# Kernel optimization log

Measured on AMD Instinct MI355X. Metric: run time of the kernel, lower is better.

The kernel has to match this reference:

```python
import jax, jax.numpy as jnp
import numpy as np

B, MB, NB, C = 4, 4096, 16384, 64

def setup_inputs() -> dict:
    key = jax.random.key(0)
    k1, k2, k3 = jax.random.split(key, 3)
    xyz = jax.random.normal(k1, (B * MB, 3), dtype=jnp.float32) * 10.0
    new_xyz = jax.random.normal(k2, (B * NB, 3), dtype=jnp.float32) * 10.0
    features = jax.random.normal(k3, (B * MB, C), dtype=jnp.float32)
    xyz_batch_cnt = jnp.full((B,), MB, dtype=jnp.int32)
    new_xyz_batch_cnt = jnp.full((B,), NB, dtype=jnp.int32)
    return {
        "xyz": xyz,
        "xyz_batch_cnt": xyz_batch_cnt,
        "new_xyz": new_xyz,
        "new_xyz_batch_cnt": new_xyz_batch_cnt,
        "features": features,
    }

def _three_nn_interp(query, known, feats):
    # query: (Nb,3), known: (Mb,3), feats: (Mb,C)
    # squared pairwise distances (Nb, Mb)
    d2 = (jnp.sum(query * query, -1, keepdims=True)
          - 2.0 * (query @ known.T)
          + jnp.sum(known * known, -1)[None, :])
    neg_d2, idx = jax.lax.top_k(-d2, 3)            # 3 nearest, (Nb,3)
    dist = jnp.sqrt(jnp.maximum(-neg_d2, 0.0))      # OpenPCDet returns sqrt(dist2)
    dist_recip = 1.0 / (dist + 1e-8)
    weight = dist_recip / jnp.sum(dist_recip, -1, keepdims=True)  # (Nb,3)
    gathered = feats[idx]                           # (Nb,3,C)
    return jnp.einsum('nkc,nk->nc', gathered, weight)

def reference(xyz, xyz_batch_cnt, new_xyz, new_xyz_batch_cnt, features):
    b = xyz_batch_cnt.shape[0]
    mb = xyz.shape[0] // b
    nb = new_xyz.shape[0] // b
    known_b = xyz.reshape(b, mb, 3)
    query_b = new_xyz.reshape(b, nb, 3)
    feats_b = features.reshape(b, mb, -1)
    out = jax.vmap(_three_nn_interp)(query_b, known_b, feats_b)  # (B,Nb,C)
    return out.reshape(b * nb, -1)
```

## Files before the change

kernel.cpp:

```cpp
#include <hip/hip_runtime.h>
#include <math.h>

#define NBIN   512
#define BEXT   64.0f
#define WSLACK 0.02f
#define AWIN   4.0f
#define BTH1   1024

__device__ __forceinline__ int bin1(float x) {
    int c = (int)floorf((x + BEXT) * 4.0f);
    return min(NBIN - 1, max(0, c));
}
__device__ __forceinline__ unsigned f2sort(float f) {
    int b = __float_as_int(f);
    return (unsigned)b ^ (0x80000000u | (unsigned)(b >> 31));
}
__device__ __forceinline__ float sort2f(unsigned u) {
    unsigned b = (u & 0x80000000u) ? (u ^ 0x80000000u) : ~u;
    return __uint_as_float(b);
}
__device__ __forceinline__ void ins3k(unsigned long long k,
                                      unsigned long long& k0,
                                      unsigned long long& k1,
                                      unsigned long long& k2) {
    const bool c0 = k < k0, c1 = k < k1, c2 = k < k2;
    k2 = c1 ? k1 : (c2 ? k : k2);
    k1 = c0 ? k0 : (c1 ? k : k1);
    k0 = c0 ? k  : k0;
}
__device__ __forceinline__ unsigned long long shfl_xor_u64(unsigned long long v, int m) {
    unsigned lo = (unsigned)v, hi = (unsigned)(v >> 32);
    lo = __shfl_xor((int)lo, m, 64);
    hi = __shfl_xor((int)hi, m, 64);
    return ((unsigned long long)hi << 32) | lo;
}

extern "C" __global__ void __launch_bounds__(BTH1)
build1d(const float* __restrict__ xyz, const float* __restrict__ nxyz,
        int mb, int nb,
        float4* __restrict__ ps, int* __restrict__ pidx,
        int* __restrict__ qord, int* __restrict__ boff,
        int* __restrict__ ovf_cnt)
{
    __shared__ int hist[NBIN];
    __shared__ int scanb[NBIN];
    const int B    = (int)gridDim.x / 2;
    const bool isQ = (int)blockIdx.x >= B;
    const int b    = isQ ? (int)blockIdx.x - B : (int)blockIdx.x;
    const int tid  = threadIdx.x;
    const int n    = isQ ? nb : mb;
    const float* P = (isQ ? nxyz : xyz) + (size_t)b * n * 3;

    if (blockIdx.x == 0 && tid < B) ovf_cnt[tid] = 0;

    if (tid < NBIN) hist[tid] = 0;
    __syncthreads();
    for (int i = tid; i < n; i += BTH1) atomicAdd(&hist[bin1(P[i * 3])], 1);
    __syncthreads();
    int h = 0;
    if (tid < NBIN) { h = hist[tid]; scanb[tid] = h; }
    __syncthreads();
    for (int off = 1; off < NBIN; off <<= 1) {
        int t = 0;
        if (tid < NBIN && tid >= off) t = scanb[tid - off];
        __syncthreads();
        if (tid < NBIN) scanb[tid] += t;
        __syncthreads();
    }
    if (tid < NBIN) {
        const int excl = scanb[tid] - h;
        if (!isQ) {
            boff[(size_t)b * (NBIN + 1) + tid] = excl;
            if (tid == NBIN - 1) boff[(size_t)b * (NBIN + 1) + NBIN] = n;
        }
        hist[tid] = excl;
    }
    __syncthreads();
    for (int i = tid; i < n; i += BTH1) {
        const float x = P[i * 3], y = P[i * 3 + 1], z = P[i * 3 + 2];
        const int c = bin1(x);
        const int pos = atomicAdd(&hist[c], 1);
        if (isQ) {
            qord[(size_t)b * nb + pos] = i;
        } else {
            float pn;
            {
#pragma clang fp contract(off)
                pn = (x * x + y * y) + z * z;
            }
            ps[(size_t)b * mb + pos]   = make_float4(x, y, z, pn);
            pidx[(size_t)b * mb + pos] = i;
        }
    }
}

#define QWA  8
#define SWA  8
#define WVBA 4
#define WTHA (WVBA * 64)
#define QPBA (WVBA * QWA)
#define CHA  64

extern "C" __global__ void __launch_bounds__(WTHA)
knn_phaseA(const float* __restrict__ nxyz, const float* __restrict__ feats,
           const int* __restrict__ qord, const int* __restrict__ boff,
           const float4* __restrict__ ps, const int* __restrict__ pidx,
           float* __restrict__ out, int* __restrict__ ovf, float* __restrict__ ovf_ub,
           int* __restrict__ ovf_cnt, int mb, int nb, int C)
{
    __shared__ float4 sP[WVBA][CHA];
    __shared__ int    sI[WVBA][CHA];

    const int tid  = threadIdx.x;
    const int w    = tid >> 6;
    const int l    = tid & 63;
    const int qi   = l & 7;
    const int side = l >> 3;
    const int wid  = blockIdx.x * WVBA + w;
    const int q0   = wid * QWA;
    const int b    = q0 / nb;

    const int qloc = qord[q0 + qi];
    const int row  = b * nb + qloc;
    const float qx = nxyz[(size_t)row * 3 + 0];
    const float qy = nxyz[(size_t)row * 3 + 1];
    const float qz = nxyz[(size_t)row * 3 + 2];
    float qq;
    {
#pragma clang fp contract(off)
        qq = (qx * qx + qy * qy) + qz * qz;
    }

    float mn = qx, mx = qx;
#pragma unroll
    for (int m = 1; m < 64; m <<= 1) {
        mn = fminf(mn, __shfl_xor(mn, m, 64));
        mx = fmaxf(mx, __shfl_xor(mx, m, 64));
    }

    const int*    boffb = boff + (size_t)b * (NBIN + 1);
    const float4* psb   = ps   + (size_t)b * mb;
    const int*    pib   = pidx + (size_t)b * mb;

    unsigned long long k0 = ~0ull, k1 = ~0ull, k2 = ~0ull;

    float4 rP;
    int    rI = 0;
    bool   rV = false;
    auto issue = [&](int base, int hi) {
        const int cand = base + l;
        rV = cand < hi;
        if (rV) { rP = psb[cand]; rI = pib[cand]; }
    };
    auto commit = [&]() {
        if (rV) { sP[w][l] = rP; sI[w][l] = rI; }
    };
    auto process = [&](int cnt) {
#pragma unroll
        for (int u = 0; u < CHA / SWA; ++u) {
            const int j = side + u * SWA;
            if (j < cnt) {
                const float4 Pt = sP[w][j];
                const int    pi = sI[w][j];
                const float dot = fmaf(qz, Pt.z, fmaf(qy, Pt.y, qx * Pt.x));
                const float d2  = fmaf(-2.0f, dot, qq) + Pt.w;
                const unsigned long long key =
                    ((unsigned long long)f2sort(d2) << 32) | (unsigned)pi;
                if (key < k2) {
                    const bool c0 = key < k0, c1 = key < k1;
                    k2 = c1 ? k1 : key;
                    k1 = c0 ? k0 : (c1 ? key : k1);
                    k0 = c0 ? key : k0;
                }
            }
        }
    };

    const int blo = bin1(mn - AWIN);
    const int bhi = bin1(mx + AWIN);
    {
        const int lo = boffb[blo], hi = boffb[bhi + 1];
        if (lo < hi) {
            issue(lo, hi);
            for (int base = lo; base < hi; base += CHA) {
                commit();
                if (base + CHA < hi) issue(base + CHA, hi);
                process(min(CHA, hi - base));
            }
        }
    }

    unsigned long long m0 = k0, m1 = k1, m2 = k2;
#pragma unroll
    for (int mk = 8; mk <= 32; mk <<= 1) {
        const unsigned long long t0 = shfl_xor_u64(m0, mk);
        const unsigned long long t1 = shfl_xor_u64(m1, mk);
        const unsigned long long t2 = shfl_xor_u64(m2, mk);
        ins3k(t0, m0, m1, m2); ins3k(t1, m0, m1, m2); ins3k(t2, m0, m1, m2);
    }

    const unsigned h2 = (unsigned)(m2 >> 32);
    const float ub = (h2 == 0xFFFFFFFFu) ? INFINITY : sort2f(h2);
    const float eL = fmaf(0.25f, (float)blo, -BEXT);
    const float eR = fmaf(0.25f, (float)(bhi + 1), -BEXT);
    const float gL = qx - eL;
    const float gR = eR - qx;
    const bool okL = (blo == 0)        || (gL * gL > ub + WSLACK);
    const bool okR = (bhi >= NBIN - 1) || (gR * gR > ub + WSLACK);
    const bool resolved = okL && okR && (h2 != 0xFFFFFFFFu);

    const bool need = (side == 0) && !resolved;
    const unsigned long long bm = __ballot(need);
    if (bm) {
        const int rank = __popcll(bm & ((1ull << l) - 1ull));
        const int tot  = __popcll(bm);
        const int lead = __ffsll((unsigned long long)bm) - 1;
        int base = 0;
        if (l == lead) base = atomicAdd(&ovf_cnt[b], tot);
        base = __shfl(base, lead, 64);
        if (need) {
            ovf[(size_t)b * nb + base + rank]    = row;
            ovf_ub[(size_t)b * nb + base + rank] = ub;
        }
    }

    const float d0  = sort2f((unsigned)(m0 >> 32));
    const float d1  = sort2f((unsigned)(m1 >> 32));
    const float d2v = sort2f((unsigned)(m2 >> 32));
    const float da = sqrtf(fmaxf(d0, 0.0f));
    const float db = sqrtf(fmaxf(d1, 0.0f));
    const float dc = sqrtf(fmaxf(d2v, 0.0f));
    const float ra = 1.0f / (da + 1e-8f);
    const float rb = 1.0f / (db + 1e-8f);
    const float rc = 1.0f / (dc + 1e-8f);
    float rs;
    {
#pragma clang fp contract(off)
        rs = (ra + rb) + rc;
    }
    const float wa = ra / rs, wb = rb / rs, wc = rc / rs;
    const int   ia = b * mb + (int)(unsigned)(m0 & 0xFFFFFFFFu);
    const int   ib = b * mb + (int)(unsigned)(m1 & 0xFFFFFFFFu);
    const int   ic = b * mb + (int)(unsigned)(m2 & 0xFFFFFFFFu);

    for (int q = 0; q < QWA; ++q) {
        if (__shfl((int)resolved, q, 64) == 0) continue;
        const float wa_ = __shfl(wa, q, 64);
        const float wb_ = __shfl(wb, q, 64);
        const float wc_ = __shfl(wc, q, 64);
        const int   ia_ = __shfl(ia, q, 64);
        const int   ib_ = __shfl(ib, q, 64);
        const int   ic_ = __shfl(ic, q, 64);
        const int   rw_ = __shfl(row, q, 64);
        const size_t ga = (size_t)ia_ * C;
        const size_t gb = (size_t)ib_ * C;
        const size_t gc = (size_t)ic_ * C;
        const size_t go = (size_t)rw_ * C;
        for (int ch = l; ch < C; ch += 64) {
            out[go + ch] = wa_ * feats[ga + ch] + wb_ * feats[gb + ch] + wc_ * feats[gc + ch];
        }
    }
}

#define WPBB 8
#define BTH2 (WPBB * 64)

extern "C" __global__ void __launch_bounds__(BTH2)
knn_phaseB2(const float* __restrict__ nxyz, const float* __restrict__ feats,
            const int* __restrict__ ovf, const float* __restrict__ ovf_ub,
            const int* __restrict__ ovf_cnt, const int* __restrict__ boff,
            const float4* __restrict__ ps, const int* __restrict__ pidx,
            float* __restrict__ out, int mb, int nb, int C)
{
    const int tid  = threadIdx.x;
    const int w    = tid >> 6;
    const int l    = tid & 63;
    const int bpb  = nb / WPBB;
    const int bb   = (int)blockIdx.x / bpb;
    const int slot = ((int)blockIdx.x % bpb) * WPBB + w;
    const int cnt  = ovf_cnt[bb];
    if (slot >= cnt) return;

    const int   row = ovf[(size_t)bb * nb + slot];
    const float ub  = ovf_ub[(size_t)bb * nb + slot];
    const float qx = nxyz[(size_t)row * 3 + 0];
    const float qy = nxyz[(size_t)row * 3 + 1];
    const float qz = nxyz[(size_t)row * 3 + 2];
    float qq;
    {
#pragma clang fp contract(off)
        qq = (qx * qx + qy * qy) + qz * qz;
    }

    int blo = 0, bhi = NBIN - 1;
    if (ub < 1e30f) {
        const float r = sqrtf(ub + 2.0f * WSLACK);
        blo = bin1(qx - r);
        bhi = bin1(qx + r);
    }
    const int*    boffb = boff + (size_t)bb * (NBIN + 1);
    const float4* psb   = ps   + (size_t)bb * mb;
    const int*    pib   = pidx + (size_t)bb * mb;
    const int lo = boffb[blo], hi = boffb[bhi + 1];

    unsigned long long k0 = ~0ull, k1 = ~0ull, k2 = ~0ull;
#pragma unroll 4
    for (int t = lo + l; t < hi; t += 64) {
        const float4 Pt = psb[t];
        const int    pi = pib[t];
        const float dot = fmaf(qz, Pt.z, fmaf(qy, Pt.y, qx * Pt.x));
        const float d2  = fmaf(-2.0f, dot, qq) + Pt.w;
        const unsigned long long key =
            ((unsigned long long)f2sort(d2) << 32) | (unsigned)pi;
        if (key < k2) {
            const bool c0 = key < k0, c1 = key < k1;
            k2 = c1 ? k1 : key;
            k1 = c0 ? k0 : (c1 ? key : k1);
            k0 = c0 ? key : k0;
        }
    }

#pragma unroll
    for (int m = 1; m < 64; m <<= 1) {
        const unsigned long long t0 = shfl_xor_u64(k0, m);
        const unsigned long long t1 = shfl_xor_u64(k1, m);
        const unsigned long long t2 = shfl_xor_u64(k2, m);
        ins3k(t0, k0, k1, k2); ins3k(t1, k0, k1, k2); ins3k(t2, k0, k1, k2);
    }

    const float d0  = sort2f((unsigned)(k0 >> 32));
    const float d1  = sort2f((unsigned)(k1 >> 32));
    const float d2v = sort2f((unsigned)(k2 >> 32));
    const float da = sqrtf(fmaxf(d0, 0.0f));
    const float db = sqrtf(fmaxf(d1, 0.0f));
    const float dc = sqrtf(fmaxf(d2v, 0.0f));
    const float ra = 1.0f / (da + 1e-8f);
    const float rb = 1.0f / (db + 1e-8f);
    const float rc = 1.0f / (dc + 1e-8f);
    float rs;
    {
#pragma clang fp contract(off)
        rs = (ra + rb) + rc;
    }
    const float wa = ra / rs, wb = rb / rs, wc = rc / rs;
    const size_t ga = (size_t)(bb * mb + (int)(unsigned)(k0 & 0xFFFFFFFFu)) * C;
    const size_t gb = (size_t)(bb * mb + (int)(unsigned)(k1 & 0xFFFFFFFFu)) * C;
    const size_t gc = (size_t)(bb * mb + (int)(unsigned)(k2 & 0xFFFFFFFFu)) * C;
    const size_t go = (size_t)row * C;
    for (int ch = l; ch < C; ch += 64) {
        out[go + ch] = wa * feats[ga + ch] + wb * feats[gb + ch] + wc * feats[gc + ch];
    }
}

#define THREADS 512
#define WAVES   8
#define RQ      2
#define QPB     128
#define CHUNK   2048

extern "C" __global__ void __launch_bounds__(THREADS)
knn3_v5(const float* __restrict__ xyz,
        const float* __restrict__ new_xyz,
        const float* __restrict__ feats,
        float* __restrict__ out,
        int mb, int nb, int C)
{
    extern __shared__ float smem[];
    float4* s_pts = (float4*)smem;
    const int tid = threadIdx.x;
    const int w   = tid >> 6;
    const int l   = tid & 63;
    const int block_q0 = blockIdx.x * QPB;
    const int batch    = block_q0 / nb;
    const int known0   = batch * mb;

    float qx[RQ], qy[RQ], qz[RQ], qq[RQ];
#pragma unroll
    for (int r = 0; r < RQ; ++r) {
        const int gq = block_q0 + r * 64 + l;
        qx[r] = new_xyz[(size_t)gq * 3 + 0];
        qy[r] = new_xyz[(size_t)gq * 3 + 1];
        qz[r] = new_xyz[(size_t)gq * 3 + 2];
        {
#pragma clang fp contract(off)
            qq[r] = (qx[r] * qx[r] + qy[r] * qy[r]) + qz[r] * qz[r];
        }
    }
    float b0[RQ], b1[RQ], b2[RQ];
    int   i0[RQ], i1[RQ], i2[RQ];
#pragma unroll
    for (int r = 0; r < RQ; ++r) {
        b0[r] = INFINITY; b1[r] = INFINITY; b2[r] = INFINITY;
        i0[r] = 0; i1[r] = 0; i2[r] = 0;
    }
    const int nch = (mb + CHUNK - 1) / CHUNK;
    for (int c = 0; c < nch; ++c) {
        const int base = c * CHUNK;
        const int cnt  = min(CHUNK, mb - base);
        if (c > 0) __syncthreads();
        const float* src = xyz + (size_t)(known0 + base) * 3;
        for (int p = tid; p < cnt; p += THREADS) {
            const float px = src[p * 3 + 0];
            const float py = src[p * 3 + 1];
            const float pz = src[p * 3 + 2];
            float pn;
            {
#pragma clang fp contract(off)
                pn = (px * px + py * py) + pz * pz;
            }
            s_pts[p] = make_float4(px, py, pz, pn);
        }
        __syncthreads();
        const int lo = (w * cnt) / WAVES;
        const int hi = ((w + 1) * cnt) / WAVES;
#pragma unroll 4
        for (int p = lo; p < hi; ++p) {
            const float4 P = s_pts[p];
            const int gp = base + p;
#pragma unroll
            for (int r = 0; r < RQ; ++r) {
                const float dot = fmaf(qz[r], P.z, fmaf(qy[r], P.y, qx[r] * P.x));
                const float d2  = fmaf(-2.0f, dot, qq[r]) + P.w;
                const bool c0 = d2 < b0[r];
                const bool c1 = d2 < b1[r];
                const bool c2 = d2 < b2[r];
                const float n0 = fminf(d2, b0[r]);
                const float n1 = __builtin_amdgcn_fmed3f(d2, b0[r], b1[r]);
                const float n2 = __builtin_amdgcn_fmed3f(d2, b1[r], b2[r]);
                const int  j0 = c0 ? gp : i0[r];
                const int  j1 = c0 ? i0[r] : (c1 ? gp : i1[r]);
                const int  j2 = c1 ? i1[r] : (c2 ? gp : i2[r]);
                b0[r] = n0; b1[r] = n1; b2[r] = n2;
                i0[r] = j0; i1[r] = j1; i2[r] = j2;
            }
        }
    }
    __syncthreads();
    float* sB  = smem;
    int*   sI  = (int*)smem + 3 * WAVES * QPB;
    float* sFW = smem + 6 * WAVES * QPB;
    int*   sFI = (int*)sFW + 3 * QPB;
#pragma unroll
    for (int r = 0; r < RQ; ++r) {
        const int qb = r * 64 + l;
        sB[(0 * WAVES + w) * QPB + qb] = b0[r];
        sB[(1 * WAVES + w) * QPB + qb] = b1[r];
        sB[(2 * WAVES + w) * QPB + qb] = b2[r];
        sI[(0 * WAVES + w) * QPB + qb] = i0[r];
        sI[(1 * WAVES + w) * QPB + qb] = i1[r];
        sI[(2 * WAVES + w) * QPB + qb] = i2[r];
    }
    __syncthreads();
    if (tid < QPB) {
        float mv0 = sB[(0 * WAVES) * QPB + tid];
        float mv1 = sB[(1 * WAVES) * QPB + tid];
        float mv2 = sB[(2 * WAVES) * QPB + tid];
        int   mi0 = sI[(0 * WAVES) * QPB + tid];
        int   mi1 = sI[(1 * WAVES) * QPB + tid];
        int   mi2 = sI[(2 * WAVES) * QPB + tid];
        for (int c = 1; c < WAVES; ++c) {
#pragma unroll
            for (int kk = 0; kk < 3; ++kk) {
                const float x  = sB[(kk * WAVES + c) * QPB + tid];
                const int   xi = sI[(kk * WAVES + c) * QPB + tid];
                const bool c0 = (x < mv0) || (x == mv0 && xi < mi0);
                const bool c1 = (x < mv1) || (x == mv1 && xi < mi1);
                const bool c2 = (x < mv2) || (x == mv2 && xi < mi2);
                const float n2 = c1 ? mv1 : (c2 ? x : mv2);
                const int   j2 = c1 ? mi1 : (c2 ? xi : mi2);
                const float n1 = c0 ? mv0 : (c1 ? x : mv1);
                const int   j1 = c0 ? mi0 : (c1 ? xi : mi1);
                const float n0 = c0 ? x : mv0;
                const int   j0 = c0 ? xi : mi0;
                mv0 = n0; mv1 = n1; mv2 = n2;
                mi0 = j0; mi1 = j1; mi2 = j2;
            }
        }
        const float da = sqrtf(fmaxf(mv0, 0.0f));
        const float db = sqrtf(fmaxf(mv1, 0.0f));
        const float dc = sqrtf(fmaxf(mv2, 0.0f));
        const float ra = 1.0f / (da + 1e-8f);
        const float rb = 1.0f / (db + 1e-8f);
        const float rc = 1.0f / (dc + 1e-8f);
        float rsum;
        {
#pragma clang fp contract(off)
            rsum = (ra + rb) + rc;
        }
        sFW[0 * QPB + tid] = ra / rsum;
        sFW[1 * QPB + tid] = rb / rsum;
        sFW[2 * QPB + tid] = rc / rsum;
        sFI[0 * QPB + tid] = known0 + mi0;
        sFI[1 * QPB + tid] = known0 + mi1;
        sFI[2 * QPB + tid] = known0 + mi2;
    }
    __syncthreads();
    const int qpw = QPB / WAVES;
    for (int j = 0; j < qpw; ++j) {
        const int qi2 = w * qpw + j;
        const float wa = sFW[0 * QPB + qi2];
        const float wb = sFW[1 * QPB + qi2];
        const float wc = sFW[2 * QPB + qi2];
        const size_t ga = (size_t)sFI[0 * QPB + qi2] * C;
        const size_t gb = (size_t)sFI[1 * QPB + qi2] * C;
        const size_t gc = (size_t)sFI[2 * QPB + qi2] * C;
        const size_t go = (size_t)(block_q0 + qi2) * C;
        for (int ch = l; ch < C; ch += 64) {
            out[go + ch] = wa * feats[ga + ch] + wb * feats[gb + ch] + wc * feats[gc + ch];
        }
    }
}

#define FQPB 256
extern "C" __global__ void __launch_bounds__(FQPB)
knn3_fallback(const float* __restrict__ xyz,
              const float* __restrict__ new_xyz,
              const float* __restrict__ feats,
              float* __restrict__ out,
              int mb, int nb, int C)
{
    extern __shared__ float4 s_pts[];
    const int tid      = threadIdx.x;
    const int block_q0 = blockIdx.x * FQPB;
    const int batch    = block_q0 / nb;
    const int known0   = batch * mb;
    for (int p = tid; p < mb; p += FQPB) {
        const float px = xyz[(size_t)(known0 + p) * 3 + 0];
        const float py = xyz[(size_t)(known0 + p) * 3 + 1];
        const float pz = xyz[(size_t)(known0 + p) * 3 + 2];
        float pn;
        {
#pragma clang fp contract(off)
            pn = (px * px + py * py) + pz * pz;
        }
        s_pts[p] = make_float4(px, py, pz, pn);
    }
    __syncthreads();
    const int gq = block_q0 + tid;
    const float qx = new_xyz[(size_t)gq * 3 + 0];
    const float qy = new_xyz[(size_t)gq * 3 + 1];
    const float qz = new_xyz[(size_t)gq * 3 + 2];
    float qq;
    {
#pragma clang fp contract(off)
        qq = (qx * qx + qy * qy) + qz * qz;
    }
    float b0 = INFINITY, b1 = INFINITY, b2 = INFINITY;
    int   i0 = 0, i1 = 0, i2 = 0;
#pragma unroll 8
    for (int p = 0; p < mb; ++p) {
        const float4 P = s_pts[p];
        const float dot = fmaf(qz, P.z, fmaf(qy, P.y, qx * P.x));
        const float d2  = fmaf(-2.0f, dot, qq) + P.w;
        const bool c0 = d2 < b0;
        const bool c1 = d2 < b1;
        const bool c2 = d2 < b2;
        b2 = c1 ? b1 : (c2 ? d2 : b2);
        i2 = c1 ? i1 : (c2 ? p  : i2);
        b1 = c0 ? b0 : (c1 ? d2 : b1);
        i1 = c0 ? i0 : (c1 ? p  : i1);
        b0 = c0 ? d2 : b0;
        i0 = c0 ? p  : i0;
    }
    const float da = sqrtf(fmaxf(b0, 0.0f));
    const float db = sqrtf(fmaxf(b1, 0.0f));
    const float dc = sqrtf(fmaxf(b2, 0.0f));
    const float ra = 1.0f / (da + 1e-8f);
    const float rb = 1.0f / (db + 1e-8f);
    const float rc = 1.0f / (dc + 1e-8f);
    float rsum;
    {
#pragma clang fp contract(off)
        rsum = (ra + rb) + rc;
    }
    const float wa = ra / rsum, wb = rb / rsum, wc = rc / rsum;
    const size_t ga = (size_t)(known0 + i0) * C;
    const size_t gb = (size_t)(known0 + i1) * C;
    const size_t gc = (size_t)(known0 + i2) * C;
    const size_t go = (size_t)gq * C;
    for (int ch = 0; ch < C; ++ch) {
        out[go + ch] = wa * feats[ga + ch] + wb * feats[gb + ch] + wc * feats[gc + ch];
    }
}

extern "C" void kernel_launch(void* const* d_in, const int* in_sizes, int n_in,
                              void* d_out, int out_size, void* d_ws, size_t ws_size,
                              hipStream_t stream) {
    const float* xyz     = (const float*)d_in[0];
    const float* new_xyz = (const float*)d_in[2];
    const float* feats   = (const float*)d_in[4];
    float*       out     = (float*)d_out;

    const int n_known = in_sizes[0] / 3;
    const int B       = in_sizes[1];
    const int n_query = in_sizes[2] / 3;
    const int C       = in_sizes[4] / n_known;
    const int mb      = n_known / B;
    const int nb      = n_query / B;

    char* wp = (char*)d_ws;
    float4* ps      = (float4*)wp;  wp += (size_t)B * mb * sizeof(float4);
    int*    pidx    = (int*)wp;     wp += (size_t)B * mb * sizeof(int);
    int*    qord    = (int*)wp;     wp += (size_t)B * nb * sizeof(int);
    int*    boff    = (int*)wp;     wp += (size_t)B * (NBIN + 1) * sizeof(int);
    int*    ovf     = (int*)wp;     wp += (size_t)B * nb * sizeof(int);
    float*  ovf_ub  = (float*)wp;   wp += (size_t)B * nb * sizeof(float);
    int*    ovf_cnt = (int*)wp;     wp += (size_t)B * sizeof(int);
    const size_t need = (size_t)(wp - (char*)d_ws);

    if (ws_size >= need && (nb % QWA) == 0 && (n_query % QPBA) == 0 &&
        (nb % WPBB) == 0 && mb >= 3 && B <= BTH1) {
        build1d<<<2 * B, BTH1, 0, stream>>>(xyz, new_xyz, mb, nb, ps, pidx, qord,
                                            boff, ovf_cnt);
        knn_phaseA<<<n_query / QPBA, WTHA, 0, stream>>>(
            new_xyz, feats, qord, boff, ps, pidx, out, ovf, ovf_ub, ovf_cnt,
            mb, nb, C);
        knn_phaseB2<<<B * (nb / WPBB), BTH2, 0, stream>>>(
            new_xyz, feats, ovf, ovf_ub, ovf_cnt, boff, ps, pidx, out, mb, nb, C);
    } else if ((nb % QPB) == 0) {
        const size_t smem_chunk = (size_t)CHUNK * sizeof(float4);
        const size_t smem_merge = (size_t)(6 * WAVES * QPB + 6 * QPB) * sizeof(float);
        const size_t shmem = smem_chunk > smem_merge ? smem_chunk : smem_merge;
        knn3_v5<<<n_query / QPB, THREADS, shmem, stream>>>(
            xyz, new_xyz, feats, out, mb, nb, C);
    } else {
        const size_t shmem = (size_t)mb * sizeof(float4);
        knn3_fallback<<<(n_query + FQPB - 1) / FQPB, FQPB, shmem, stream>>>(
            xyz, new_xyz, feats, out, mb, nb, C);
    }
}
```

Measured before the change: 96.13 us.

## Split 1D binning build into sliced histogram, scan, and scatter kernels

Replaces the single-block-per-batch counting-sort build with three kernels: per-slice shared-memory histograms across 64 slices per batch, a column scan that turns slice histograms into global offsets, and a per-slice scatter. Until now only 2*B blocks (8) did the build, which left most of the GPU idle; now 2*B*64 blocks share the work. The cost is two extra kernel launches and additional workspace for the slice histograms, and the old path is kept as a fallback when workspace is too small. Ordering within a bin now depends on atomic order inside each slice, which is nondeterministic, as it likely was before.

```diff
diff --git a/kernel.cpp b/kernel.cpp
--- a/kernel.cpp
+++ b/kernel.cpp
@@ -5,6 +5,7 @@
 #define BEXT   64.0f
 #define WSLACK 0.02f
 #define AWIN   4.0f
+#define SLC    64
 #define BTH1   1024
 
 __device__ __forceinline__ int bin1(float x) {
@@ -33,6 +34,101 @@
     lo = __shfl_xor((int)lo, m, 64);
     hi = __shfl_xor((int)hi, m, 64);
     return ((unsigned long long)hi << 32) | lo;
+}
+
+extern "C" __global__ void __launch_bounds__(256)
+k_shist(const float* __restrict__ xyz, const float* __restrict__ nxyz,
+        int B, int mb, int nb,
+        int* __restrict__ hP, int* __restrict__ hQ, int* __restrict__ ovf_cnt)
+{
+    __shared__ int hist[NBIN];
+    const int bid = (int)blockIdx.x;
+    const bool isQ = bid >= B * SLC;
+    const int rb = isQ ? bid - B * SLC : bid;
+    const int b = rb / SLC, s = rb % SLC;
+    const int n = isQ ? nb : mb;
+    const int len = (n + SLC - 1) / SLC;
+    const int beg = s * len, end = min(n, beg + len);
+    const float* P = (isQ ? nxyz : xyz) + (size_t)b * n * 3;
+    const int tid = threadIdx.x;
+
+    if (bid == 0 && tid < B) ovf_cnt[tid] = 0;
+
+    for (int i = tid; i < NBIN; i += 256) hist[i] = 0;
+    __syncthreads();
+    for (int i = beg + tid; i < end; i += 256) atomicAdd(&hist[bin1(P[i * 3])], 1);
+    __syncthreads();
+    int* dst = (isQ ? hQ : hP) + ((size_t)b * SLC + s) * NBIN;
+    for (int i = tid; i < NBIN; i += 256) dst[i] = hist[i];
+}
+
+extern "C" __global__ void __launch_bounds__(NBIN)
+k_sscan(int* __restrict__ hP, int* __restrict__ hQ,
+        int* __restrict__ boff, int B, int mb)
+{
+    __shared__ int sc[NBIN];
+    const bool isQ = (int)blockIdx.x >= B;
+    const int b = isQ ? (int)blockIdx.x - B : (int)blockIdx.x;
+    int* h = (isQ ? hQ : hP) + (size_t)b * SLC * NBIN;
+    const int c = threadIdx.x;
+
+    int run = 0;
+    for (int s = 0; s < SLC; ++s) {
+        const int v = h[s * NBIN + c];
+        h[s * NBIN + c] = run;
+        run += v;
+    }
+    sc[c] = run;
+    __syncthreads();
+    for (int off = 1; off < NBIN; off <<= 1) {
+        const int t = (c >= off) ? sc[c - off] : 0;
+        __syncthreads();
+        sc[c] += t;
+        __syncthreads();
+    }
+    const int excl = sc[c] - run;
+    for (int s = 0; s < SLC; ++s) h[s * NBIN + c] += excl;
+    if (!isQ) {
+        boff[(size_t)b * (NBIN + 1) + c] = excl;
+        if (c == NBIN - 1) boff[(size_t)b * (NBIN + 1) + NBIN] = mb;
+    }
+}
+
+extern "C" __global__ void __launch_bounds__(256)
+k_sscat(const float* __restrict__ xyz, const float* __restrict__ nxyz,
+        int B, int mb, int nb,
+        const int* __restrict__ hP, const int* __restrict__ hQ,
+        float4* __restrict__ ps, int* __restrict__ pidx, int* __restrict__ qord)
+{
+    __shared__ int cur[NBIN];
+    const int bid = (int)blockIdx.x;
+    const bool isQ = bid >= B * SLC;
+    const int rb = isQ ? bid - B * SLC : bid;
+    const int b = rb / SLC, s = rb % SLC;
+    const int n = isQ ? nb : mb;
+    const int len = (n + SLC - 1) / SLC;
+    const int beg = s * len, end = min(n, beg + len);
+    const float* P = (isQ ? nxyz : xyz) + (size_t)b * n * 3;
+    const int tid = threadIdx.x;
+    const int* src = (isQ ? hQ : hP) + ((size_t)b * SLC + s) * NBIN;
+
+    for (int i = tid; i < NBIN; i += 256) cur[i] = src[i];
+    __syncthreads();
+    for (int i = beg + tid; i < end; i += 256) {
+        const float x = P[i * 3], y = P[i * 3 + 1], z = P[i * 3 + 2];
+        const int pos = atomicAdd(&cur[bin1(x)], 1);
+        if (isQ) {
+            qord[(size_t)b * nb + pos] = i;
+        } else {
+            float pn;
+            {
+#pragma clang fp contract(off)
+                pn = (x * x + y * y) + z * z;
+            }
+            ps[(size_t)b * mb + pos]   = make_float4(x, y, z, pn);
+            pidx[(size_t)b * mb + pos] = i;
+        }
+    }
 }
 
 extern "C" __global__ void __launch_bounds__(BTH1)
@@ -606,10 +702,25 @@
     int*    ovf     = (int*)wp;     wp += (size_t)B * nb * sizeof(int);
     float*  ovf_ub  = (float*)wp;   wp += (size_t)B * nb * sizeof(float);
     int*    ovf_cnt = (int*)wp;     wp += (size_t)B * sizeof(int);
-    const size_t need = (size_t)(wp - (char*)d_ws);
-
-    if (ws_size >= need && (nb % QWA) == 0 && (n_query % QPBA) == 0 &&
-        (nb % WPBB) == 0 && mb >= 3 && B <= BTH1) {
+    const size_t need_base = (size_t)(wp - (char*)d_ws);
+    int*    hP      = (int*)wp;     wp += (size_t)B * SLC * NBIN * sizeof(int);
+    int*    hQ      = (int*)wp;     wp += (size_t)B * SLC * NBIN * sizeof(int);
+    const size_t need_slice = (size_t)(wp - (char*)d_ws);
+
+    const bool ok_shape = (nb % QWA) == 0 && (n_query % QPBA) == 0 &&
+                          (nb % WPBB) == 0 && mb >= 3 && B <= 256;
+
+    if (ok_shape && ws_size >= need_slice) {
+        k_shist<<<2 * B * SLC, 256, 0, stream>>>(xyz, new_xyz, B, mb, nb, hP, hQ, ovf_cnt);
+        k_sscan<<<2 * B, NBIN, 0, stream>>>(hP, hQ, boff, B, mb);
+        k_sscat<<<2 * B * SLC, 256, 0, stream>>>(xyz, new_xyz, B, mb, nb, hP, hQ,
+                                                 ps, pidx, qord);
+        knn_phaseA<<<n_query / QPBA, WTHA, 0, stream>>>(
+            new_xyz, feats, qord, boff, ps, pidx, out, ovf, ovf_ub, ovf_cnt,
+            mb, nb, C);
+        knn_phaseB2<<<B * (nb / WPBB), BTH2, 0, stream>>>(
+            new_xyz, feats, ovf, ovf_ub, ovf_cnt, boff, ps, pidx, out, mb, nb, C);
+    } else if (ok_shape && ws_size >= need_base && B <= BTH1) {
         build1d<<<2 * B, BTH1, 0, stream>>>(xyz, new_xyz, mb, nb, ps, pidx, qord,
                                             boff, ovf_cnt);
         knn_phaseA<<<n_query / QPBA, WTHA, 0, stream>>>(
```

Measured after the change: 97.00 us. Within noise of the previous version (+0.9%).
